# Optimization experiments

Hardware: AMD Instinct MI355X
Metric: run time of the kernel (lower is better)

The kernel has to match this reference:

```python
import jax, jax.numpy as jnp
import numpy as np

LN_EPS = 1e-5

def setup_inputs() -> dict:
    key = jax.random.key(0)
    ks = jax.random.split(key, 8)
    B, d, var_dim, hidden = 1024, 32, 64, 256
    in_dim = d * var_dim
    causal_vars = jax.random.normal(ks[0], (B, d, var_dim), dtype=jnp.float32)
    adj_soft = jax.random.uniform(ks[1], (d, d), dtype=jnp.float32)
    # Per-variable MLP params (stacked along leading d axis), torch-default-like init scale
    s1 = 1.0 / np.sqrt(in_dim)
    s2 = 1.0 / np.sqrt(hidden)
    W1 = jax.random.uniform(ks[2], (d, in_dim, hidden), minval=-s1, maxval=s1, dtype=jnp.float32)
    b1 = jax.random.uniform(ks[3], (d, hidden), minval=-s1, maxval=s1, dtype=jnp.float32)
    W2 = jax.random.uniform(ks[4], (d, hidden, var_dim), minval=-s2, maxval=s2, dtype=jnp.float32)
    b2 = jax.random.uniform(ks[5], (d, var_dim), minval=-s2, maxval=s2, dtype=jnp.float32)
    gamma = jnp.ones((d, var_dim), dtype=jnp.float32)
    beta = jnp.zeros((d, var_dim), dtype=jnp.float32)
    return {"causal_vars": causal_vars, "adj_soft": adj_soft, "W1": W1, "b1": b1,
            "W2": W2, "b2": b2, "gamma": gamma, "beta": beta}

def reference(causal_vars, adj_soft, W1, b1, W2, b2, gamma, beta):
    B, d, var_dim = causal_vars.shape
    # masked parent input for equation i: adj_soft[i, j] * causal_vars[b, j, :]
    # shape (B, d_eq, d_parent, var_dim) -> flatten parents: (B, d, d*var_dim)
    x = adj_soft[None, :, :, None] * causal_vars[:, None, :, :]
    x = x.reshape(B, d, d * var_dim)
    # grouped 2-layer MLP, distinct weights per variable i
    h = jnp.einsum('bik,ikh->bih', x, W1) + b1[None]
    h = jax.nn.gelu(h, approximate=False)
    y = jnp.einsum('bih,ihv->biv', h, W2) + b2[None]
    # LayerNorm over var_dim with per-variable affine params
    mu = jnp.mean(y, axis=-1, keepdims=True)
    var = jnp.var(y, axis=-1, keepdims=True)
    y = (y - mu) * jax.lax.rsqrt(var + LN_EPS)
    return y * gamma[None] + beta[None]  # (B, d, var_dim)
```

## Files before the change

### kernel.cpp

```cpp
#include <hip/hip_runtime.h>
#include <hip/hip_bf16.h>

typedef __bf16 bf16_t;
typedef __bf16 bf16x8 __attribute__((ext_vector_type(8)));
typedef float f32x4 __attribute__((ext_vector_type(4)));

#define NB 1024
#define ND 32
#define VD 64
#define NH 256
#define NK 2048

#define OFF_A    0
#define OFF_W1T  (4u*1024u*1024u)
#define OFF_W2T  (36u*1024u*1024u)

#define GLD16(gsrc, ldst) \
  __builtin_amdgcn_global_load_lds((const __attribute__((address_space(1))) void*)(gsrc), \
                                   (__attribute__((address_space(3))) void*)(ldst), 16, 0, 0)

__global__ __launch_bounds__(256) void prep_kernel(
    const float* __restrict__ cv, const float* __restrict__ adj,
    const float* __restrict__ W1, const float* __restrict__ W2,
    bf16_t* __restrict__ A, bf16_t* __restrict__ W1T, bf16_t* __restrict__ W2T)
{
  __shared__ float Ls[64 * 67];
  int bx = blockIdx.x;
  int tid = threadIdx.x;
  if (bx < 4096) {
    int i = bx >> 7;
    int rem = bx & 127;
    int k0 = (rem >> 2) * 64;
    int h0 = (rem & 3) * 64;
    float a = adj[i * 32 + (k0 >> 6)];
    int rrow = tid >> 4, c4 = (tid & 15) * 4;
#pragma unroll
    for (int p = 0; p < 4; ++p) {
      int row = p * 16 + rrow;
      const float* src = W1 + ((size_t)(i * 2048 + k0 + row)) * 256 + h0 + c4;
      float4 v = *(const float4*)src;
#pragma unroll
      for (int j = 0; j < 4; ++j) Ls[row * 67 + c4 + j] = a * ((const float*)&v)[j];
    }
    __syncthreads();
#pragma unroll
    for (int p = 0; p < 2; ++p) {
      int u = p * 256 + tid;
      int h = u >> 3, c8 = u & 7;
      bf16x8 o;
#pragma unroll
      for (int j = 0; j < 8; ++j) o[j] = (bf16_t)Ls[(c8 * 8 + j) * 67 + h];
      *(bf16x8*)(W1T + ((size_t)(i * 256 + h0 + h)) * 2048 + k0 + c8 * 8) = o;
    }
  } else if (bx < 5120) {
    int t = (bx - 4096) * 256 + tid;
    const float4* s = (const float4*)cv + (size_t)t * 2;
    float4 v0 = s[0], v1 = s[1];
    bf16x8 o;
    o[0] = (bf16_t)v0.x; o[1] = (bf16_t)v0.y; o[2] = (bf16_t)v0.z; o[3] = (bf16_t)v0.w;
    o[4] = (bf16_t)v1.x; o[5] = (bf16_t)v1.y; o[6] = (bf16_t)v1.z; o[7] = (bf16_t)v1.w;
    *(bf16x8*)(A + (size_t)t * 8) = o;
  } else {
    int t = (bx - 5120) * 256 + tid;
    int i = t >> 11;
    int rem = t & 2047;
    int h8 = rem >> 6;
    int v = rem & 63;
    const float* src = W2 + ((size_t)(i * 256 + h8 * 8)) * 64 + v;
    bf16x8 o;
#pragma unroll
    for (int r = 0; r < 8; ++r) o[r] = (bf16_t)src[(size_t)r * 64];
    *(bf16x8*)(W2T + ((size_t)(i * 64 + v)) * 256 + h8 * 8) = o;
  }
}

__global__ __launch_bounds__(256, 2) void sem_main_kernel(
    const bf16_t* __restrict__ A, const bf16_t* __restrict__ W1T,
    const bf16_t* __restrict__ W2T,
    const float* __restrict__ b1, const float* __restrict__ b2,
    const float* __restrict__ gamma, const float* __restrict__ beta,
    float* __restrict__ out)
{
  __shared__ char smem[61440];

  int p = blockIdx.x;
  int L = (p & 7) * 64 + (p >> 3);
  int i = L >> 4;
  int brow = (L & 15) * 64;

  int tid = threadIdx.x;
  int lane = tid & 63;
  int wid = tid >> 6;
  int lhi = lane >> 4;
  int llo = lane & 15;

  const bf16_t* W1Ti = W1T + (size_t)i * 256 * 2048;

  int arow = tid >> 2, ac = tid & 3;
  const bf16_t* aSrc = A + (size_t)(brow + arow) * 2048 + (ac ^ ((arow >> 1) & 3)) * 8;
  const bf16_t* bSrc0 = W1Ti + (size_t)arow * 2048 + (ac ^ ((arow >> 1) & 3)) * 8;
  const bf16_t* bSrc1 = W1Ti + (size_t)(64 + arow) * 2048 + (ac ^ (((64 + arow) >> 1) & 3)) * 8;
  const bf16_t* bSrc2 = W1Ti + (size_t)(128 + arow) * 2048 + (ac ^ (((128 + arow) >> 1) & 3)) * 8;
  const bf16_t* bSrc3 = W1Ti + (size_t)(192 + arow) * 2048 + (ac ^ (((192 + arow) >> 1) & 3)) * 8;
  int ldsW = wid * 1024;

  auto stage = [&](int b, int kt) {
    char* base = smem + b * 20480;
    GLD16(aSrc + kt * 32, base + ldsW);
    GLD16(bSrc0 + kt * 32, base + 4096 + ldsW);
    GLD16(bSrc1 + kt * 32, base + 8192 + ldsW);
    GLD16(bSrc2 + kt * 32, base + 12288 + ldsW);
    GLD16(bSrc3 + kt * 32, base + 16384 + ldsW);
  };

  int aOff[4], bOff[4];
#pragma unroll
  for (int m = 0; m < 4; ++m) {
    int row = m * 16 + llo;
    aOff[m] = row * 64 + ((lhi ^ ((row >> 1) & 3)) * 16);
  }
#pragma unroll
  for (int n = 0; n < 4; ++n) {
    int row = wid * 64 + n * 16 + llo;
    bOff[n] = 4096 + row * 64 + ((lhi ^ ((row >> 1) & 3)) * 16);
  }

  f32x4 acc[4][4];
#pragma unroll
  for (int m = 0; m < 4; ++m)
#pragma unroll
    for (int n = 0; n < 4; ++n) acc[m][n] = (f32x4){0.f, 0.f, 0.f, 0.f};

  auto compute = [&](int b) {
    const char* base = smem + b * 20480;
    bf16x8 af[4], bfr[4];
#pragma unroll
    for (int m = 0; m < 4; ++m) af[m] = *(const bf16x8*)(base + aOff[m]);
#pragma unroll
    for (int n = 0; n < 4; ++n) bfr[n] = *(const bf16x8*)(base + bOff[n]);
    __builtin_amdgcn_s_setprio(1);
#pragma unroll
    for (int m = 0; m < 4; ++m)
#pragma unroll
      for (int n = 0; n < 4; ++n)
        acc[m][n] = __builtin_amdgcn_mfma_f32_16x16x32_bf16(af[m], bfr[n], acc[m][n], 0, 0, 0);
    __builtin_amdgcn_s_setprio(0);
  };

  asm volatile("" ::: "memory");
  stage(0, 0); stage(1, 1);
  int bc = 0, bs = 2;
  for (int t = 0; t < 62; ++t) {
    asm volatile("s_waitcnt vmcnt(5) lgkmcnt(0)" ::: "memory");
    __builtin_amdgcn_s_barrier();
    asm volatile("" ::: "memory");
    stage(bs, t + 2);
    compute(bc);
    bc = (bc == 2) ? 0 : bc + 1;
    bs = (bs == 2) ? 0 : bs + 1;
  }
  asm volatile("s_waitcnt vmcnt(5) lgkmcnt(0)" ::: "memory");
  __builtin_amdgcn_s_barrier();
  asm volatile("" ::: "memory");
  compute(2);
  asm volatile("s_waitcnt vmcnt(0) lgkmcnt(0)" ::: "memory");
  __builtin_amdgcn_s_barrier();
  asm volatile("" ::: "memory");
  compute(0);
  __syncthreads();

  bf16_t* Hs = (bf16_t*)smem;
  float bias[4];
#pragma unroll
  for (int n = 0; n < 4; ++n) bias[n] = b1[i * 256 + wid * 64 + n * 16 + llo];
#pragma unroll
  for (int m = 0; m < 4; ++m) {
#pragma unroll
    for (int n = 0; n < 4; ++n) {
      int col = wid * 64 + n * 16 + llo;
#pragma unroll
      for (int r = 0; r < 4; ++r) {
        int row = m * 16 + lhi * 4 + r;
        float x = acc[m][n][r] + bias[n];
        float gl = 0.5f * x * (1.0f + erff(x * 0.70710678118654752f));
        Hs[row * 264 + col] = (bf16_t)gl;
      }
    }
  }
  __syncthreads();

  f32x4 acc2[4];
#pragma unroll
  for (int n = 0; n < 4; ++n) acc2[n] = (f32x4){0.f, 0.f, 0.f, 0.f};
  const bf16_t* W2Ti = W2T + (size_t)i * 64 * 256;
#pragma unroll
  for (int kk = 0; kk < 8; ++kk) {
    int k = kk * 32 + lhi * 8;
    bf16x8 af = *(const bf16x8*)(Hs + (wid * 16 + llo) * 264 + k);
#pragma unroll
    for (int n = 0; n < 4; ++n) {
      bf16x8 bfr = *(const bf16x8*)(W2Ti + (size_t)(n * 16 + llo) * 256 + k);
      acc2[n] = __builtin_amdgcn_mfma_f32_16x16x32_bf16(af, bfr, acc2[n], 0, 0, 0);
    }
  }

  float b2v[4], gam[4], bet[4];
#pragma unroll
  for (int n = 0; n < 4; ++n) {
    int v = n * 16 + llo;
    b2v[n] = b2[i * 64 + v];
    gam[n] = gamma[i * 64 + v];
    bet[n] = beta[i * 64 + v];
  }
#pragma unroll
  for (int r = 0; r < 4; ++r) {
    float yv[4], s = 0.f, sq = 0.f;
#pragma unroll
    for (int n = 0; n < 4; ++n) {
      yv[n] = acc2[n][r] + b2v[n];
      s += yv[n];
      sq += yv[n] * yv[n];
    }
#pragma unroll
    for (int off = 1; off < 16; off <<= 1) {
      s += __shfl_xor(s, off, 64);
      sq += __shfl_xor(sq, off, 64);
    }
    float mu = s * (1.0f / 64.0f);
    float var = sq * (1.0f / 64.0f) - mu * mu;
    float rstd = rsqrtf(var + 1e-5f);
    int row = brow + wid * 16 + lhi * 4 + r;
    float* op = out + ((size_t)row * 32 + i) * 64;
#pragma unroll
    for (int n = 0; n < 4; ++n)
      op[n * 16 + llo] = (yv[n] - mu) * rstd * gam[n] + bet[n];
  }
}

extern "C" void kernel_launch(void* const* d_in, const int* in_sizes, int n_in,
                              void* d_out, int out_size, void* d_ws, size_t ws_size,
                              hipStream_t stream) {
  const float* cv    = (const float*)d_in[0];
  const float* adj   = (const float*)d_in[1];
  const float* W1    = (const float*)d_in[2];
  const float* b1    = (const float*)d_in[3];
  const float* W2    = (const float*)d_in[4];
  const float* b2    = (const float*)d_in[5];
  const float* gamma = (const float*)d_in[6];
  const float* beta  = (const float*)d_in[7];
  float* out = (float*)d_out;

  bf16_t* Abf  = (bf16_t*)((char*)d_ws + OFF_A);
  bf16_t* W1T  = (bf16_t*)((char*)d_ws + OFF_W1T);
  bf16_t* W2T  = (bf16_t*)((char*)d_ws + OFF_W2T);

  prep_kernel<<<5376, 256, 0, stream>>>(cv, adj, W1, W2, Abf, W1T, W2T);
  sem_main_kernel<<<512, 256, 0, stream>>>(Abf, W1T, W2T, b1, b2, gamma, beta, out);
}
```

Measured before the change: 80.39 us.

## Split main GEMM block across eight waves with 2x4 warp tiling

Doubles the main kernel's block to 512 threads, arranging the waves as a 2x4 grid so each wave computes a 32x64 output tile instead of 64x64. The tile staging is spread across the extra waves, with only the first four loading the A tile, and each wave waits on its own outstanding-load count. The aim is more waves in flight per CU to hide memory and MFMA latency. In exchange, each wave reuses its loaded fragments less, half the waves sit idle during the second GEMM and LayerNorm, and the launch-bounds change limits registers per wave.

```diff
diff --git a/kernel.cpp b/kernel.cpp
--- a/kernel.cpp
+++ b/kernel.cpp
@@ -74,7 +74,7 @@
   }
 }
 
-__global__ __launch_bounds__(256, 2) void sem_main_kernel(
+__global__ __launch_bounds__(512, 4) void sem_main_kernel(
     const bf16_t* __restrict__ A, const bf16_t* __restrict__ W1T,
     const bf16_t* __restrict__ W2T,
     const float* __restrict__ b1, const float* __restrict__ b2,
@@ -91,67 +91,71 @@
   int tid = threadIdx.x;
   int lane = tid & 63;
   int wid = tid >> 6;
+  int wr = wid >> 2;
+  int wc = wid & 3;
   int lhi = lane >> 4;
   int llo = lane & 15;
 
   const bf16_t* W1Ti = W1T + (size_t)i * 256 * 2048;
 
   int arow = tid >> 2, ac = tid & 3;
-  const bf16_t* aSrc = A + (size_t)(brow + arow) * 2048 + (ac ^ ((arow >> 1) & 3)) * 8;
-  const bf16_t* bSrc0 = W1Ti + (size_t)arow * 2048 + (ac ^ ((arow >> 1) & 3)) * 8;
-  const bf16_t* bSrc1 = W1Ti + (size_t)(64 + arow) * 2048 + (ac ^ (((64 + arow) >> 1) & 3)) * 8;
-  const bf16_t* bSrc2 = W1Ti + (size_t)(128 + arow) * 2048 + (ac ^ (((128 + arow) >> 1) & 3)) * 8;
-  const bf16_t* bSrc3 = W1Ti + (size_t)(192 + arow) * 2048 + (ac ^ (((192 + arow) >> 1) & 3)) * 8;
+  int sc0 = ac ^ ((arow >> 1) & 3);
+  const bf16_t* aSrc  = A + (size_t)(brow + arow) * 2048 + sc0 * 8;
+  const bf16_t* bSrc0 = W1Ti + (size_t)arow * 2048 + sc0 * 8;
+  const bf16_t* bSrc1 = W1Ti + (size_t)(128 + arow) * 2048 + sc0 * 8;
   int ldsW = wid * 1024;
 
   auto stage = [&](int b, int kt) {
     char* base = smem + b * 20480;
-    GLD16(aSrc + kt * 32, base + ldsW);
-    GLD16(bSrc0 + kt * 32, base + 4096 + ldsW);
-    GLD16(bSrc1 + kt * 32, base + 8192 + ldsW);
-    GLD16(bSrc2 + kt * 32, base + 12288 + ldsW);
-    GLD16(bSrc3 + kt * 32, base + 16384 + ldsW);
+    if (wid < 4) GLD16(aSrc + (size_t)kt * 32, base + ldsW);
+    GLD16(bSrc0 + (size_t)kt * 32, base + 4096 + ldsW);
+    GLD16(bSrc1 + (size_t)kt * 32, base + 12288 + ldsW);
   };
 
-  int aOff[4], bOff[4];
-#pragma unroll
-  for (int m = 0; m < 4; ++m) {
-    int row = m * 16 + llo;
+  int aOff[2], bOff[4];
+#pragma unroll
+  for (int m = 0; m < 2; ++m) {
+    int row = wr * 32 + m * 16 + llo;
     aOff[m] = row * 64 + ((lhi ^ ((row >> 1) & 3)) * 16);
   }
 #pragma unroll
   for (int n = 0; n < 4; ++n) {
-    int row = wid * 64 + n * 16 + llo;
+    int row = wc * 64 + n * 16 + llo;
     bOff[n] = 4096 + row * 64 + ((lhi ^ ((row >> 1) & 3)) * 16);
   }
 
-  f32x4 acc[4][4];
-#pragma unroll
-  for (int m = 0; m < 4; ++m)
+  f32x4 acc[2][4];
+#pragma unroll
+  for (int m = 0; m < 2; ++m)
 #pragma unroll
     for (int n = 0; n < 4; ++n) acc[m][n] = (f32x4){0.f, 0.f, 0.f, 0.f};
 
   auto compute = [&](int b) {
     const char* base = smem + b * 20480;
-    bf16x8 af[4], bfr[4];
-#pragma unroll
-    for (int m = 0; m < 4; ++m) af[m] = *(const bf16x8*)(base + aOff[m]);
+    bf16x8 af[2], bfr[4];
+#pragma unroll
+    for (int m = 0; m < 2; ++m) af[m] = *(const bf16x8*)(base + aOff[m]);
 #pragma unroll
     for (int n = 0; n < 4; ++n) bfr[n] = *(const bf16x8*)(base + bOff[n]);
     __builtin_amdgcn_s_setprio(1);
 #pragma unroll
-    for (int m = 0; m < 4; ++m)
+    for (int m = 0; m < 2; ++m)
 #pragma unroll
       for (int n = 0; n < 4; ++n)
         acc[m][n] = __builtin_amdgcn_mfma_f32_16x16x32_bf16(af[m], bfr[n], acc[m][n], 0, 0, 0);
     __builtin_amdgcn_s_setprio(0);
   };
 
+#define WAIT_OWN_TILE() do { \
+    if (wid < 4) asm volatile("s_waitcnt vmcnt(3) lgkmcnt(0)" ::: "memory"); \
+    else         asm volatile("s_waitcnt vmcnt(2) lgkmcnt(0)" ::: "memory"); \
+  } while (0)
+
   asm volatile("" ::: "memory");
   stage(0, 0); stage(1, 1);
   int bc = 0, bs = 2;
   for (int t = 0; t < 62; ++t) {
-    asm volatile("s_waitcnt vmcnt(5) lgkmcnt(0)" ::: "memory");
+    WAIT_OWN_TILE();
     __builtin_amdgcn_s_barrier();
     asm volatile("" ::: "memory");
     stage(bs, t + 2);
@@ -159,7 +163,7 @@
     bc = (bc == 2) ? 0 : bc + 1;
     bs = (bs == 2) ? 0 : bs + 1;
   }
-  asm volatile("s_waitcnt vmcnt(5) lgkmcnt(0)" ::: "memory");
+  WAIT_OWN_TILE();
   __builtin_amdgcn_s_barrier();
   asm volatile("" ::: "memory");
   compute(2);
@@ -172,15 +176,15 @@
   bf16_t* Hs = (bf16_t*)smem;
   float bias[4];
 #pragma unroll
-  for (int n = 0; n < 4; ++n) bias[n] = b1[i * 256 + wid * 64 + n * 16 + llo];
-#pragma unroll
-  for (int m = 0; m < 4; ++m) {
+  for (int n = 0; n < 4; ++n) bias[n] = b1[i * 256 + wc * 64 + n * 16 + llo];
+#pragma unroll
+  for (int m = 0; m < 2; ++m) {
 #pragma unroll
     for (int n = 0; n < 4; ++n) {
-      int col = wid * 64 + n * 16 + llo;
+      int col = wc * 64 + n * 16 + llo;
 #pragma unroll
       for (int r = 0; r < 4; ++r) {
-        int row = m * 16 + lhi * 4 + r;
+        int row = wr * 32 + m * 16 + lhi * 4 + r;
         float x = acc[m][n][r] + bias[n];
         float gl = 0.5f * x * (1.0f + erff(x * 0.70710678118654752f));
         Hs[row * 264 + col] = (bf16_t)gl;
@@ -189,51 +193,52 @@
   }
   __syncthreads();
 
-  f32x4 acc2[4];
-#pragma unroll
-  for (int n = 0; n < 4; ++n) acc2[n] = (f32x4){0.f, 0.f, 0.f, 0.f};
-  const bf16_t* W2Ti = W2T + (size_t)i * 64 * 256;
-#pragma unroll
-  for (int kk = 0; kk < 8; ++kk) {
-    int k = kk * 32 + lhi * 8;
-    bf16x8 af = *(const bf16x8*)(Hs + (wid * 16 + llo) * 264 + k);
+  if (wid < 4) {
+    f32x4 acc2[4];
+#pragma unroll
+    for (int n = 0; n < 4; ++n) acc2[n] = (f32x4){0.f, 0.f, 0.f, 0.f};
+    const bf16_t* W2Ti = W2T + (size_t)i * 64 * 256;
+#pragma unroll
+    for (int kk = 0; kk < 8; ++kk) {
+      int k = kk * 32 + lhi * 8;
+      bf16x8 af = *(const bf16x8*)(Hs + (wid * 16 + llo) * 264 + k);
+#pragma unroll
+      for (int n = 0; n < 4; ++n) {
+        bf16x8 bfr = *(const bf16x8*)(W2Ti + (size_t)(n * 16 + llo) * 256 + k);
+        acc2[n] = __builtin_amdgcn_mfma_f32_16x16x32_bf16(af, bfr, acc2[n], 0, 0, 0);
+      }
+    }
+    float b2v[4], gam[4], bet[4];
 #pragma unroll
     for (int n = 0; n < 4; ++n) {
-      bf16x8 bfr = *(const bf16x8*)(W2Ti + (size_t)(n * 16 + llo) * 256 + k);
-      acc2[n] = __builtin_amdgcn_mfma_f32_16x16x32_bf16(af, bfr, acc2[n], 0, 0, 0);
-    }
-  }
-
-  float b2v[4], gam[4], bet[4];
-#pragma unroll
-  for (int n = 0; n < 4; ++n) {
-    int v = n * 16 + llo;
-    b2v[n] = b2[i * 64 + v];
-    gam[n] = gamma[i * 64 + v];
-    bet[n] = beta[i * 64 + v];
-  }
-#pragma unroll
-  for (int r = 0; r < 4; ++r) {
-    float yv[4], s = 0.f, sq = 0.f;
-#pragma unroll
-    for (int n = 0; n < 4; ++n) {
-      yv[n] = acc2[n][r] + b2v[n];
-      s += yv[n];
-      sq += yv[n] * yv[n];
-    }
-#pragma unroll
-    for (int off = 1; off < 16; off <<= 1) {
-      s += __shfl_xor(s, off, 64);
-      sq += __shfl_xor(sq, off, 64);
-    }
-    float mu = s * (1.0f / 64.0f);
-    float var = sq * (1.0f / 64.0f) - mu * mu;
-    float rstd = rsqrtf(var + 1e-5f);
-    int row = brow + wid * 16 + lhi * 4 + r;
-    float* op = out + ((size_t)row * 32 + i) * 64;
-#pragma unroll
-    for (int n = 0; n < 4; ++n)
-      op[n * 16 + llo] = (yv[n] - mu) * rstd * gam[n] + bet[n];
+      int v = n * 16 + llo;
+      b2v[n] = b2[i * 64 + v];
+      gam[n] = gamma[i * 64 + v];
+      bet[n] = beta[i * 64 + v];
+    }
+#pragma unroll
+    for (int r = 0; r < 4; ++r) {
+      float yv[4], s = 0.f, sq = 0.f;
+#pragma unroll
+      for (int n = 0; n < 4; ++n) {
+        yv[n] = acc2[n][r] + b2v[n];
+        s += yv[n];
+        sq += yv[n] * yv[n];
+      }
+#pragma unroll
+      for (int off = 1; off < 16; off <<= 1) {
+        s += __shfl_xor(s, off, 64);
+        sq += __shfl_xor(sq, off, 64);
+      }
+      float mu = s * (1.0f / 64.0f);
+      float var = sq * (1.0f / 64.0f) - mu * mu;
+      float rstd = rsqrtf(var + 1e-5f);
+      int row = brow + wid * 16 + lhi * 4 + r;
+      float* op = out + ((size_t)row * 32 + i) * 64;
+#pragma unroll
+      for (int n = 0; n < 4; ++n)
+        op[n * 16 + llo] = (yv[n] - mu) * rstd * gam[n] + bet[n];
+    }
   }
 }
 
@@ -255,5 +260,5 @@
   bf16_t* W2T  = (bf16_t*)((char*)d_ws + OFF_W2T);
 
   prep_kernel<<<5376, 256, 0, stream>>>(cv, adj, W1, W2, Abf, W1T, W2T);
-  sem_main_kernel<<<512, 256, 0, stream>>>(Abf, W1T, W2T, b1, b2, gamma, beta, out);
+  sem_main_kernel<<<512, 512, 0, stream>>>(Abf, W1T, W2T, b1, b2, gamma, beta, out);
 }
```

Result: faster. 78.50 us (-2.4%).

## Halve batch tile, single-buffer K=64 stages, raise occupancy to four blocks

Applied to the files above, without the earlier changes.

The main GEMM kernel now tiles 32 batch rows per block instead of 64 and launches 1024 blocks with launch bounds allowing four blocks per CU. Each K step stages 64 wide in a single LDS buffer, replacing the triple-buffered async pipeline with plain syncthreads around each stage. Waves are split 2x2 over rows and hidden columns, and only two waves do the second GEMM and LayerNorm. The aim is more parallelism and latency hiding through occupancy. The cost is losing explicit load/compute overlap within a block, re-reading W1 twice as often per equation, and leaving half the waves idle in the epilogue.

```diff
diff --git a/kernel.cpp b/kernel.cpp
--- a/kernel.cpp
+++ b/kernel.cpp
@@ -74,166 +74,138 @@
   }
 }
 
-__global__ __launch_bounds__(256, 2) void sem_main_kernel(
+__global__ __launch_bounds__(256, 4) void sem_main_kernel(
     const bf16_t* __restrict__ A, const bf16_t* __restrict__ W1T,
     const bf16_t* __restrict__ W2T,
     const float* __restrict__ b1, const float* __restrict__ b2,
     const float* __restrict__ gamma, const float* __restrict__ beta,
     float* __restrict__ out)
 {
-  __shared__ char smem[61440];
+  __shared__ char smem[36864];
 
   int p = blockIdx.x;
-  int L = (p & 7) * 64 + (p >> 3);
-  int i = L >> 4;
-  int brow = (L & 15) * 64;
+  int L = (p & 7) * 128 + (p >> 3);
+  int i = L >> 5;
+  int brow = (L & 31) * 32;
 
   int tid = threadIdx.x;
   int lane = tid & 63;
   int wid = tid >> 6;
+  int wr = wid >> 1;
+  int wc = wid & 1;
   int lhi = lane >> 4;
   int llo = lane & 15;
 
   const bf16_t* W1Ti = W1T + (size_t)i * 256 * 2048;
 
-  int arow = tid >> 2, ac = tid & 3;
-  const bf16_t* aSrc = A + (size_t)(brow + arow) * 2048 + (ac ^ ((arow >> 1) & 3)) * 8;
-  const bf16_t* bSrc0 = W1Ti + (size_t)arow * 2048 + (ac ^ ((arow >> 1) & 3)) * 8;
-  const bf16_t* bSrc1 = W1Ti + (size_t)(64 + arow) * 2048 + (ac ^ (((64 + arow) >> 1) & 3)) * 8;
-  const bf16_t* bSrc2 = W1Ti + (size_t)(128 + arow) * 2048 + (ac ^ (((128 + arow) >> 1) & 3)) * 8;
-  const bf16_t* bSrc3 = W1Ti + (size_t)(192 + arow) * 2048 + (ac ^ (((192 + arow) >> 1) & 3)) * 8;
+  int arow = tid >> 3, ac = tid & 7;
+  int sc0 = ac ^ (arow & 7);
+  const bf16_t* aSrc = A + (size_t)(brow + arow) * 2048 + sc0 * 8;
+  const bf16_t* bSrc = W1Ti + (size_t)arow * 2048 + sc0 * 8;
   int ldsW = wid * 1024;
 
-  auto stage = [&](int b, int kt) {
-    char* base = smem + b * 20480;
-    GLD16(aSrc + kt * 32, base + ldsW);
-    GLD16(bSrc0 + kt * 32, base + 4096 + ldsW);
-    GLD16(bSrc1 + kt * 32, base + 8192 + ldsW);
-    GLD16(bSrc2 + kt * 32, base + 12288 + ldsW);
-    GLD16(bSrc3 + kt * 32, base + 16384 + ldsW);
+  auto stage = [&](int kt) {
+    GLD16(aSrc + (size_t)kt * 64, smem + ldsW);
+#pragma unroll
+    for (int r = 0; r < 8; ++r)
+      GLD16(bSrc + (size_t)r * 65536 + (size_t)kt * 64, smem + 4096 + r * 4096 + ldsW);
   };
 
-  int aOff[4], bOff[4];
-#pragma unroll
-  for (int m = 0; m < 4; ++m) {
-    int row = m * 16 + llo;
-    aOff[m] = row * 64 + ((lhi ^ ((row >> 1) & 3)) * 16);
-  }
-#pragma unroll
-  for (int n = 0; n < 4; ++n) {
-    int row = wid * 64 + n * 16 + llo;
-    bOff[n] = 4096 + row * 64 + ((lhi ^ ((row >> 1) & 3)) * 16);
-  }
-
-  f32x4 acc[4][4];
-#pragma unroll
-  for (int m = 0; m < 4; ++m)
-#pragma unroll
-    for (int n = 0; n < 4; ++n) acc[m][n] = (f32x4){0.f, 0.f, 0.f, 0.f};
-
-  auto compute = [&](int b) {
-    const char* base = smem + b * 20480;
-    bf16x8 af[4], bfr[4];
-#pragma unroll
-    for (int m = 0; m < 4; ++m) af[m] = *(const bf16x8*)(base + aOff[m]);
-#pragma unroll
-    for (int n = 0; n < 4; ++n) bfr[n] = *(const bf16x8*)(base + bOff[n]);
-    __builtin_amdgcn_s_setprio(1);
-#pragma unroll
-    for (int m = 0; m < 4; ++m)
+  int arf = wr * 16 + llo;
+  int aOff[2];
+#pragma unroll
+  for (int kk = 0; kk < 2; ++kk)
+    aOff[kk] = arf * 128 + (((kk * 4 + lhi) ^ (arf & 7)) * 16);
+  int bOff[2][8];
+#pragma unroll
+  for (int n = 0; n < 8; ++n) {
+    int brf = wc * 128 + n * 16 + llo;
+#pragma unroll
+    for (int kk = 0; kk < 2; ++kk)
+      bOff[kk][n] = 4096 + brf * 128 + (((kk * 4 + lhi) ^ (brf & 7)) * 16);
+  }
+
+  f32x4 acc[8];
+#pragma unroll
+  for (int n = 0; n < 8; ++n) acc[n] = (f32x4){0.f, 0.f, 0.f, 0.f};
+
+  stage(0);
+  for (int t = 0; t < 32; ++t) {
+    __syncthreads();
+#pragma unroll
+    for (int kk = 0; kk < 2; ++kk) {
+      bf16x8 af = *(const bf16x8*)(smem + aOff[kk]);
+#pragma unroll
+      for (int n = 0; n < 8; ++n) {
+        bf16x8 bfr = *(const bf16x8*)(smem + bOff[kk][n]);
+        acc[n] = __builtin_amdgcn_mfma_f32_16x16x32_bf16(af, bfr, acc[n], 0, 0, 0);
+      }
+    }
+    __syncthreads();
+    if (t < 31) stage(t + 1);
+  }
+
+  bf16_t* Hs = (bf16_t*)smem;
+#pragma unroll
+  for (int n = 0; n < 8; ++n) {
+    int col = wc * 128 + n * 16 + llo;
+    float bias = b1[i * 256 + col];
+#pragma unroll
+    for (int r = 0; r < 4; ++r) {
+      int row = wr * 16 + lhi * 4 + r;
+      float x = acc[n][r] + bias;
+      float gl = 0.5f * x * (1.0f + erff(x * 0.70710678118654752f));
+      Hs[row * 264 + col] = (bf16_t)gl;
+    }
+  }
+  __syncthreads();
+
+  if (wid < 2) {
+    f32x4 acc2[4];
+#pragma unroll
+    for (int n = 0; n < 4; ++n) acc2[n] = (f32x4){0.f, 0.f, 0.f, 0.f};
+    const bf16_t* W2Ti = W2T + (size_t)i * 64 * 256;
+#pragma unroll
+    for (int kk = 0; kk < 8; ++kk) {
+      int k = kk * 32 + lhi * 8;
+      bf16x8 af = *(const bf16x8*)(Hs + (wid * 16 + llo) * 264 + k);
+#pragma unroll
+      for (int n = 0; n < 4; ++n) {
+        bf16x8 bfr = *(const bf16x8*)(W2Ti + (size_t)(n * 16 + llo) * 256 + k);
+        acc2[n] = __builtin_amdgcn_mfma_f32_16x16x32_bf16(af, bfr, acc2[n], 0, 0, 0);
+      }
+    }
+    float b2v[4], gam[4], bet[4];
+#pragma unroll
+    for (int n = 0; n < 4; ++n) {
+      int v = n * 16 + llo;
+      b2v[n] = b2[i * 64 + v];
+      gam[n] = gamma[i * 64 + v];
+      bet[n] = beta[i * 64 + v];
+    }
+#pragma unroll
+    for (int r = 0; r < 4; ++r) {
+      float yv[4], s = 0.f, sq = 0.f;
+#pragma unroll
+      for (int n = 0; n < 4; ++n) {
+        yv[n] = acc2[n][r] + b2v[n];
+        s += yv[n];
+        sq += yv[n] * yv[n];
+      }
+#pragma unroll
+      for (int off = 1; off < 16; off <<= 1) {
+        s += __shfl_xor(s, off, 64);
+        sq += __shfl_xor(sq, off, 64);
+      }
+      float mu = s * (1.0f / 64.0f);
+      float var = sq * (1.0f / 64.0f) - mu * mu;
+      float rstd = rsqrtf(var + 1e-5f);
+      int row = brow + wid * 16 + lhi * 4 + r;
+      float* op = out + ((size_t)row * 32 + i) * 64;
 #pragma unroll
       for (int n = 0; n < 4; ++n)
-        acc[m][n] = __builtin_amdgcn_mfma_f32_16x16x32_bf16(af[m], bfr[n], acc[m][n], 0, 0, 0);
-    __builtin_amdgcn_s_setprio(0);
-  };
-
-  asm volatile("" ::: "memory");
-  stage(0, 0); stage(1, 1);
-  int bc = 0, bs = 2;
-  for (int t = 0; t < 62; ++t) {
-    asm volatile("s_waitcnt vmcnt(5) lgkmcnt(0)" ::: "memory");
-    __builtin_amdgcn_s_barrier();
-    asm volatile("" ::: "memory");
-    stage(bs, t + 2);
-    compute(bc);
-    bc = (bc == 2) ? 0 : bc + 1;
-    bs = (bs == 2) ? 0 : bs + 1;
-  }
-  asm volatile("s_waitcnt vmcnt(5) lgkmcnt(0)" ::: "memory");
-  __builtin_amdgcn_s_barrier();
-  asm volatile("" ::: "memory");
-  compute(2);
-  asm volatile("s_waitcnt vmcnt(0) lgkmcnt(0)" ::: "memory");
-  __builtin_amdgcn_s_barrier();
-  asm volatile("" ::: "memory");
-  compute(0);
-  __syncthreads();
-
-  bf16_t* Hs = (bf16_t*)smem;
-  float bias[4];
-#pragma unroll
-  for (int n = 0; n < 4; ++n) bias[n] = b1[i * 256 + wid * 64 + n * 16 + llo];
-#pragma unroll
-  for (int m = 0; m < 4; ++m) {
-#pragma unroll
-    for (int n = 0; n < 4; ++n) {
-      int col = wid * 64 + n * 16 + llo;
-#pragma unroll
-      for (int r = 0; r < 4; ++r) {
-        int row = m * 16 + lhi * 4 + r;
-        float x = acc[m][n][r] + bias[n];
-        float gl = 0.5f * x * (1.0f + erff(x * 0.70710678118654752f));
-        Hs[row * 264 + col] = (bf16_t)gl;
-      }
-    }
-  }
-  __syncthreads();
-
-  f32x4 acc2[4];
-#pragma unroll
-  for (int n = 0; n < 4; ++n) acc2[n] = (f32x4){0.f, 0.f, 0.f, 0.f};
-  const bf16_t* W2Ti = W2T + (size_t)i * 64 * 256;
-#pragma unroll
-  for (int kk = 0; kk < 8; ++kk) {
-    int k = kk * 32 + lhi * 8;
-    bf16x8 af = *(const bf16x8*)(Hs + (wid * 16 + llo) * 264 + k);
-#pragma unroll
-    for (int n = 0; n < 4; ++n) {
-      bf16x8 bfr = *(const bf16x8*)(W2Ti + (size_t)(n * 16 + llo) * 256 + k);
-      acc2[n] = __builtin_amdgcn_mfma_f32_16x16x32_bf16(af, bfr, acc2[n], 0, 0, 0);
-    }
-  }
-
-  float b2v[4], gam[4], bet[4];
-#pragma unroll
-  for (int n = 0; n < 4; ++n) {
-    int v = n * 16 + llo;
-    b2v[n] = b2[i * 64 + v];
-    gam[n] = gamma[i * 64 + v];
-    bet[n] = beta[i * 64 + v];
-  }
-#pragma unroll
-  for (int r = 0; r < 4; ++r) {
-    float yv[4], s = 0.f, sq = 0.f;
-#pragma unroll
-    for (int n = 0; n < 4; ++n) {
-      yv[n] = acc2[n][r] + b2v[n];
-      s += yv[n];
-      sq += yv[n] * yv[n];
-    }
-#pragma unroll
-    for (int off = 1; off < 16; off <<= 1) {
-      s += __shfl_xor(s, off, 64);
-      sq += __shfl_xor(sq, off, 64);
-    }
-    float mu = s * (1.0f / 64.0f);
-    float var = sq * (1.0f / 64.0f) - mu * mu;
-    float rstd = rsqrtf(var + 1e-5f);
-    int row = brow + wid * 16 + lhi * 4 + r;
-    float* op = out + ((size_t)row * 32 + i) * 64;
-#pragma unroll
-    for (int n = 0; n < 4; ++n)
-      op[n * 16 + llo] = (yv[n] - mu) * rstd * gam[n] + bet[n];
+        op[n * 16 + llo] = (yv[n] - mu) * rstd * gam[n] + bet[n];
+    }
   }
 }
 
@@ -255,5 +227,5 @@
   bf16_t* W2T  = (bf16_t*)((char*)d_ws + OFF_W2T);
 
   prep_kernel<<<5376, 256, 0, stream>>>(cv, adj, W1, W2, Abf, W1T, W2T);
-  sem_main_kernel<<<512, 256, 0, stream>>>(Abf, W1T, W2T, b1, b2, gamma, beta, out);
+  sem_main_kernel<<<1024, 256, 0, stream>>>(Abf, W1T, W2T, b1, b2, gamma, beta, out);
 }
```

Result: slower. 87.52 us (+8.9%).
